# Kernel tuning notes

Measured on AMD Instinct MI355X. Metric: run time of the kernel, lower is better.

## Reference

```python
import jax, jax.numpy as jnp
import numpy as np

USER_COUNT = 100_000
ITEM_COUNT = 50_000
N_NODES = USER_COUNT + ITEM_COUNT
EMB = 128
N_LAYERS = 3
NNZ = 1_600_000
BATCH = 4096


def setup_inputs() -> dict:
    key = jax.random.key(0)
    k1, k2, k3, k4, k5 = jax.random.split(key, 5)
    # xavier-uniform-ish init scale for the embedding tables
    bound = float(np.sqrt(6.0 / (USER_COUNT + EMB)))
    user_emb = jax.random.uniform(k1, (USER_COUNT, EMB), jnp.float32, -bound, bound)
    bound_i = float(np.sqrt(6.0 / (ITEM_COUNT + EMB)))
    item_emb = jax.random.uniform(k2, (ITEM_COUNT, EMB), jnp.float32, -bound_i, bound_i)
    # random COO normalized adjacency (stand-in for scipy norm_adj)
    rng = np.random.default_rng(0)
    adj_rows = jnp.asarray(rng.integers(0, N_NODES, NNZ), dtype=jnp.int32)
    adj_cols = jnp.asarray(rng.integers(0, N_NODES, NNZ), dtype=jnp.int32)
    # values ~ 1/avg_degree so repeated SpMM stays numerically tame
    adj_vals = jnp.asarray(rng.random(NNZ, dtype=np.float32) * 0.1)
    users = jax.random.randint(k3, (BATCH,), 0, USER_COUNT, dtype=jnp.int64)
    items = jax.random.randint(k4, (BATCH,), 0, ITEM_COUNT, dtype=jnp.int64)
    return {
        "user_emb": user_emb,
        "item_emb": item_emb,
        "adj_vals": adj_vals,
        "adj_rows": adj_rows,
        "adj_cols": adj_cols,
        "users": users,
        "items": items,
    }


def _spmm(vals, rows, cols, x):
    # sparse [N,N] @ dense [N,D] via gather + segment_sum
    gathered = vals[:, None] * x[cols]  # [nnz, D]
    return jax.ops.segment_sum(gathered, rows, num_segments=N_NODES)


def reference(user_emb, item_emb, adj_vals, adj_rows, adj_cols, users, items):
    ego = jnp.concatenate([user_emb, item_emb], axis=0)  # [N, D]
    acc = ego  # running sum over layer outputs (fused stack+mean)
    for _ in range(N_LAYERS):
        ego = _spmm(adj_vals, adj_rows, adj_cols, ego)
        acc = acc + ego
    mean_emb = acc / (N_LAYERS + 1)
    user_out = mean_emb[users]
    item_out = mean_emb[USER_COUNT + items]
    return (user_out, item_out)
```

## Files before the change

kernel.cpp:

```cpp
#include <hip/hip_runtime.h>
#include <hip/hip_bf16.h>

#define USER_COUNT 100000
#define ITEM_COUNT 50000
#define N_NODES    (USER_COUNT + ITEM_COUNT)
#define EMB        128
#define NNZ        1600000
#define BATCH      4096

#define BSHIFT  10
#define BROWS   (1 << BSHIFT)
#define NBUCKET ((N_NODES + BROWS - 1) >> BSHIFT)
#define CAP     12288
#define TILE    4096

typedef unsigned int uint32;
typedef unsigned long long uint64;


__device__ __forceinline__ float bflo(uint32 p) { return __uint_as_float(p << 16); }
__device__ __forceinline__ float bfhi(uint32 p) { return __uint_as_float(p & 0xffff0000u); }
__device__ __forceinline__ uint32 bf16of(float a)
{
    uint32 u = __float_as_uint(a);
    return (u + 0x7fffu + ((u >> 16) & 1u)) >> 16;
}
__device__ __forceinline__ uint32 bf16pair(float a, float b)
{
    uint32 ua = __float_as_uint(a);
    uint32 ub = __float_as_uint(b);
    ua = (ua + 0x7fffu + ((ua >> 16) & 1u)) >> 16;
    ub = (ub + 0x7fffu + ((ub >> 16) & 1u)) & 0xffff0000u;
    return ua | ub;
}

__device__ __forceinline__ float dec14(uint32 rec)
{
    return __uint_as_float((((rec >> 28) + 108u) << 23) | (((rec >> 18) & 0x3FFu) << 13));
}
__device__ __forceinline__ uint32 enc14(uint32 b16)
{
    uint32 exp = (b16 >> 7) & 0xFFu;
    uint32 m7  = b16 & 0x7Fu;
    return (exp >= 108u) ? (((exp - 108u) << 10) | (m7 << 3)) : 0u;
}

__global__ void to_bf16(const float* __restrict__ user_emb,
                        const float* __restrict__ item_emb,
                        uint32* __restrict__ ego,
                        int* __restrict__ cursor,
                        uint32* __restrict__ mark)
{
    size_t t = (size_t)blockIdx.x * blockDim.x + threadIdx.x;
    if (t < NBUCKET) cursor[t] = 0;
    if (t < (N_NODES + 3) / 4) mark[t] = 0;
    size_t base = t * 8;
    if (base >= (size_t)N_NODES * EMB) return;
    const size_t user_elems = (size_t)USER_COUNT * EMB;
    const float* src = (base < user_elems) ? user_emb + base
                                           : item_emb + (base - user_elems);
    float4 a = *(const float4*)(src);
    float4 b = *(const float4*)(src + 4);
    uint32* dst = ego + base / 2;
    dst[0] = bf16pair(a.x, a.y);
    dst[1] = bf16pair(a.z, a.w);
    dst[2] = bf16pair(b.x, b.y);
    dst[3] = bf16pair(b.z, b.w);
}

__global__ __launch_bounds__(256)
void bin_coarse(const int* __restrict__ rows,
                const int* __restrict__ cols,
                const float* __restrict__ vals,
                int* __restrict__ cursor,
                uint64* __restrict__ binned)
{
    __shared__ int cnt[NBUCKET];
    __shared__ int offs[NBUCKET];
    __shared__ int base[NBUCKET];
    __shared__ int cur[NBUCKET];
    __shared__ int wsum[4];
    __shared__ uint64 stage[TILE];
    int t = threadIdx.x;
    int tileBase = blockIdx.x * TILE;
    int tileCount = min(TILE, NNZ - tileBase);

    for (int i = t; i < NBUCKET; i += 256) { cnt[i] = 0; cur[i] = 0; }
    __syncthreads();
    for (int i = t; i < tileCount; i += 256)
        atomicAdd(&cnt[rows[tileBase + i] >> BSHIFT], 1);
    __syncthreads();
    {
        int lane = t & 63, wid = t >> 6;
        int mine = (t < NBUCKET) ? cnt[t] : 0;
        int v = mine;
        #pragma unroll
        for (int off = 1; off <= 32; off <<= 1) {
            int u = __shfl_up(v, off, 64);
            if (lane >= off) v += u;
        }
        if (lane == 63) wsum[wid] = v;
        __syncthreads();
        int add = 0;
        for (int w = 0; w < wid; ++w) add += wsum[w];
        if (t < NBUCKET) offs[t] = v + add - mine;
    }
    if (t < NBUCKET) base[t] = atomicAdd(&cursor[t], cnt[t]);
    __syncthreads();
    for (int i = t; i < tileCount; i += 256) {
        int r = rows[tileBase + i];
        int c = cols[tileBase + i];
        float v = vals[tileBase + i];
        int b = r >> BSHIFT;
        int p = offs[b] + atomicAdd(&cur[b], 1);
        stage[p] = ((uint64)bf16of(v) << 36) | ((uint64)(uint32)r << 18) | (uint32)c;
    }
    __syncthreads();
    for (int i = t; i < tileCount; i += 256) {
        uint64 rec = stage[i];
        int r = (int)((rec >> 18) & 0x3FFFFu);
        int b = r >> BSHIFT;
        int dest = b * CAP + base[b] + (i - offs[b]);
        binned[dest] = rec;
    }
}

__global__ __launch_bounds__(1024)
void bin_fine(const int* __restrict__ cursor,
              const uint64* __restrict__ binned,
              uint32* __restrict__ row_info4,
              uint32* __restrict__ csr4)
{
    __shared__ int hist[BROWS];
    __shared__ int wsum[16];
    int b = blockIdx.x;
    int t = threadIdx.x;
    int lo = b * CAP;
    int hi = lo + cursor[b];

    hist[t] = 0;
    __syncthreads();
    for (int i = lo + t; i < hi; i += 1024) {
        int r = (int)((binned[i] >> 18) & 0x3FFFFu);
        atomicAdd(&hist[r & (BROWS - 1)], 1);
    }
    __syncthreads();
    int myVal = hist[t];
    int lane = t & 63, wid = t >> 6;
    int v = myVal;
    #pragma unroll
    for (int off = 1; off <= 32; off <<= 1) {
        int u = __shfl_up(v, off, 64);
        if (lane >= off) v += u;
    }
    if (lane == 63) wsum[wid] = v;
    __syncthreads();
    if (wid == 0 && lane < 16) {
        int s = wsum[lane];
        #pragma unroll
        for (int off = 1; off <= 8; off <<= 1) {
            int u = __shfl_up(s, off, 64);
            if (lane >= off) s += u;
        }
        wsum[lane] = s;
    }
    __syncthreads();
    int waveExcl = (wid == 0) ? 0 : wsum[wid - 1];
    int excl = waveExcl + v - myVal;
    int grow = (b << BSHIFT) + t;
    if (grow < N_NODES)
        row_info4[grow] = (uint32)(lo + excl) | ((uint32)myVal << 24);
    hist[t] = excl;
    __syncthreads();
    for (int i = lo + t; i < hi; i += 1024) {
        uint64 rec = binned[i];
        uint32 c = (uint32)(rec & 0x3FFFFu);
        int r = (int)((rec >> 18) & 0x3FFFFu);
        uint32 b16 = (uint32)(rec >> 36);
        int pos = lo + atomicAdd(&hist[r & (BROWS - 1)], 1);
        csr4[pos] = (enc14(b16) << 18) | c;
    }
}

__global__ void mark_needed(const uint32* __restrict__ row_info4,
                            const uint32* __restrict__ csr4,
                            const int* __restrict__ users,
                            const int* __restrict__ items,
                            unsigned char* __restrict__ mark)
{
    int b = blockIdx.x * blockDim.x + threadIdx.x;
    if (b >= 2 * BATCH) return;
    int node = (b < BATCH) ? users[b] : USER_COUNT + items[b - BATCH];
    mark[node] = 1;
    uint32 info = row_info4[node];
    int s = (int)(info & 0xFFFFFFu);
    int e = s + (int)(info >> 24);
    for (int k = s; k < e; ++k)
        mark[csr4[k] & 0x3FFFFu] = 1;
}

__global__ __launch_bounds__(256, 8)
void spmm_bf16(const uint32* __restrict__ row_info4,
               const uint32* __restrict__ csr4,
               const uint32* __restrict__ x,
               uint32* __restrict__ y)
{
    int half = threadIdx.x >> 5;
    int r = blockIdx.x * 8 + half;
    if (r >= N_NODES) return;
    int j = (threadIdx.x & 31) * 2;
    uint32 info = row_info4[r];
    int s = (int)(info & 0xFFFFFFu);
    int e = s + (int)(info >> 24);
    float4 acc = { 0.f, 0.f, 0.f, 0.f };
    for (int k = s; k < e; k += 4) {
        int i1 = (k + 1 < e) ? k + 1 : e - 1;
        int i2 = (k + 2 < e) ? k + 2 : e - 1;
        int i3 = (k + 3 < e) ? k + 3 : e - 1;
        uint32 r0 = csr4[k];
        uint32 r1 = csr4[i1];
        uint32 r2 = csr4[i2];
        uint32 r3 = csr4[i3];
        float v0 = dec14(r0);
        float v1 = (k + 1 < e) ? dec14(r1) : 0.f;
        float v2 = (k + 2 < e) ? dec14(r2) : 0.f;
        float v3 = (k + 3 < e) ? dec14(r3) : 0.f;
        uint2 g0 = *(const uint2*)(x + (size_t)(r0 & 0x3FFFFu) * (EMB / 2) + j);
        uint2 g1 = *(const uint2*)(x + (size_t)(r1 & 0x3FFFFu) * (EMB / 2) + j);
        uint2 g2 = *(const uint2*)(x + (size_t)(r2 & 0x3FFFFu) * (EMB / 2) + j);
        uint2 g3 = *(const uint2*)(x + (size_t)(r3 & 0x3FFFFu) * (EMB / 2) + j);
        acc.x += v0 * bflo(g0.x) + v1 * bflo(g1.x) + v2 * bflo(g2.x) + v3 * bflo(g3.x);
        acc.y += v0 * bfhi(g0.x) + v1 * bfhi(g1.x) + v2 * bfhi(g2.x) + v3 * bfhi(g3.x);
        acc.z += v0 * bflo(g0.y) + v1 * bflo(g1.y) + v2 * bflo(g2.y) + v3 * bflo(g3.y);
        acc.w += v0 * bfhi(g0.y) + v1 * bfhi(g1.y) + v2 * bfhi(g2.y) + v3 * bfhi(g3.y);
    }
    uint2 o;
    o.x = bf16pair(acc.x, acc.y);
    o.y = bf16pair(acc.z, acc.w);
    *(uint2*)(y + (size_t)r * (EMB / 2) + j) = o;
}

__global__ __launch_bounds__(256, 8)
void spmm_bf16_masked(const uint32* __restrict__ row_info4,
                      const uint32* __restrict__ csr4,
                      const uint32* __restrict__ x,
                      const unsigned char* __restrict__ mark,
                      uint32* __restrict__ y)
{
    int half = threadIdx.x >> 5;
    int r = blockIdx.x * 8 + half;
    if (r >= N_NODES) return;
    if (!mark[r]) return;
    int j = (threadIdx.x & 31) * 2;
    uint32 info = row_info4[r];
    int s = (int)(info & 0xFFFFFFu);
    int e = s + (int)(info >> 24);
    float4 acc = { 0.f, 0.f, 0.f, 0.f };
    for (int k = s; k < e; k += 4) {
        int i1 = (k + 1 < e) ? k + 1 : e - 1;
        int i2 = (k + 2 < e) ? k + 2 : e - 1;
        int i3 = (k + 3 < e) ? k + 3 : e - 1;
        uint32 r0 = csr4[k];
        uint32 r1 = csr4[i1];
        uint32 r2 = csr4[i2];
        uint32 r3 = csr4[i3];
        float v0 = dec14(r0);
        float v1 = (k + 1 < e) ? dec14(r1) : 0.f;
        float v2 = (k + 2 < e) ? dec14(r2) : 0.f;
        float v3 = (k + 3 < e) ? dec14(r3) : 0.f;
        uint2 g0 = *(const uint2*)(x + (size_t)(r0 & 0x3FFFFu) * (EMB / 2) + j);
        uint2 g1 = *(const uint2*)(x + (size_t)(r1 & 0x3FFFFu) * (EMB / 2) + j);
        uint2 g2 = *(const uint2*)(x + (size_t)(r2 & 0x3FFFFu) * (EMB / 2) + j);
        uint2 g3 = *(const uint2*)(x + (size_t)(r3 & 0x3FFFFu) * (EMB / 2) + j);
        acc.x += v0 * bflo(g0.x) + v1 * bflo(g1.x) + v2 * bflo(g2.x) + v3 * bflo(g3.x);
        acc.y += v0 * bfhi(g0.x) + v1 * bfhi(g1.x) + v2 * bfhi(g2.x) + v3 * bfhi(g3.x);
        acc.z += v0 * bflo(g0.y) + v1 * bflo(g1.y) + v2 * bflo(g2.y) + v3 * bflo(g3.y);
        acc.w += v0 * bfhi(g0.y) + v1 * bfhi(g1.y) + v2 * bfhi(g2.y) + v3 * bfhi(g3.y);
    }
    uint2 o;
    o.x = bf16pair(acc.x, acc.y);
    o.y = bf16pair(acc.z, acc.w);
    *(uint2*)(y + (size_t)r * (EMB / 2) + j) = o;
}

__global__ void spmm_final(const uint32* __restrict__ row_info4,
                           const uint32* __restrict__ csr4,
                           const uint32* __restrict__ buf0,
                           const uint32* __restrict__ buf1,
                           const float* __restrict__ user_emb,
                           const float* __restrict__ item_emb,
                           const int*   __restrict__ users,
                           const int*   __restrict__ items,
                           float* __restrict__ out)
{
    int half = threadIdx.x >> 5;
    int b = blockIdx.x * 8 + half;
    if (b >= 2 * BATCH) return;
    int node;
    const float* ego0;
    if (b < BATCH) {
        node = users[b];
        ego0 = user_emb + (size_t)node * EMB;
    } else {
        int it = items[b - BATCH];
        node = USER_COUNT + it;
        ego0 = item_emb + (size_t)it * EMB;
    }
    int j2 = (threadIdx.x & 31) * 2;
    int j4 = (threadIdx.x & 31) * 4;
    uint32 info = row_info4[node];
    int s = (int)(info & 0xFFFFFFu);
    int e = s + (int)(info >> 24);
    float4 acc = { 0.f, 0.f, 0.f, 0.f };
    for (int k = s; k < e; k += 4) {
        int i1 = (k + 1 < e) ? k + 1 : e - 1;
        int i2 = (k + 2 < e) ? k + 2 : e - 1;
        int i3 = (k + 3 < e) ? k + 3 : e - 1;
        uint32 r0 = csr4[k];
        uint32 r1 = csr4[i1];
        uint32 r2 = csr4[i2];
        uint32 r3 = csr4[i3];
        float v0 = dec14(r0);
        float v1 = (k + 1 < e) ? dec14(r1) : 0.f;
        float v2 = (k + 2 < e) ? dec14(r2) : 0.f;
        float v3 = (k + 3 < e) ? dec14(r3) : 0.f;
        uint2 g0 = *(const uint2*)(buf1 + (size_t)(r0 & 0x3FFFFu) * (EMB / 2) + j2);
        uint2 g1 = *(const uint2*)(buf1 + (size_t)(r1 & 0x3FFFFu) * (EMB / 2) + j2);
        uint2 g2 = *(const uint2*)(buf1 + (size_t)(r2 & 0x3FFFFu) * (EMB / 2) + j2);
        uint2 g3 = *(const uint2*)(buf1 + (size_t)(r3 & 0x3FFFFu) * (EMB / 2) + j2);
        acc.x += v0 * bflo(g0.x) + v1 * bflo(g1.x) + v2 * bflo(g2.x) + v3 * bflo(g3.x);
        acc.y += v0 * bfhi(g0.x) + v1 * bfhi(g1.x) + v2 * bfhi(g2.x) + v3 * bfhi(g3.x);
        acc.z += v0 * bflo(g0.y) + v1 * bflo(g1.y) + v2 * bflo(g2.y) + v3 * bflo(g3.y);
        acc.w += v0 * bfhi(g0.y) + v1 * bfhi(g1.y) + v2 * bfhi(g2.y) + v3 * bfhi(g3.y);
    }
    float4 a0 = *(const float4*)(ego0 + j4);
    uint2 b0 = *(const uint2*)(buf0 + (size_t)node * (EMB / 2) + j2);
    uint2 b1 = *(const uint2*)(buf1 + (size_t)node * (EMB / 2) + j2);
    float4 o;
    o.x = 0.25f * (a0.x + bflo(b0.x) + bflo(b1.x) + acc.x);
    o.y = 0.25f * (a0.y + bfhi(b0.x) + bfhi(b1.x) + acc.y);
    o.z = 0.25f * (a0.z + bflo(b0.y) + bflo(b1.y) + acc.z);
    o.w = 0.25f * (a0.w + bfhi(b0.y) + bfhi(b1.y) + acc.w);
    *(float4*)(out + (size_t)b * EMB + j4) = o;
}

extern "C" void kernel_launch(void* const* d_in, const int* in_sizes, int n_in,
                              void* d_out, int out_size, void* d_ws, size_t ws_size,
                              hipStream_t stream) {
    const float* user_emb = (const float*)d_in[0];
    const float* item_emb = (const float*)d_in[1];
    const float* adj_vals = (const float*)d_in[2];
    const int*   adj_rows = (const int*)d_in[3];
    const int*   adj_cols = (const int*)d_in[4];
    const int*   users    = (const int*)d_in[5];
    const int*   items    = (const int*)d_in[6];
    float* out = (float*)d_out;

    const size_t node_pairs = (size_t)N_NODES * (EMB / 2);
    char* p = (char*)d_ws;
    uint32* ego  = (uint32*)p;               p += node_pairs * sizeof(uint32);
    uint32* buf0 = (uint32*)p;               p += node_pairs * sizeof(uint32);
    uint32* buf1 = (uint32*)p;               p += node_pairs * sizeof(uint32);
    int* cursor       = (int*)p;             p += ((NBUCKET + 3) & ~3) * sizeof(int);
    uint32* mark      = (uint32*)p;          p += ((N_NODES + 63) & ~63);
    uint32* row_info4 = (uint32*)p;          p += (size_t)N_NODES * sizeof(uint32);
    uint64* binned    = (uint64*)p;          p += (size_t)NBUCKET * CAP * sizeof(uint64);
    uint32* csr4      = (uint32*)p;

    {
        size_t total = ((size_t)N_NODES * EMB) / 8;
        to_bf16<<<(int)((total + 255) / 256), 256, 0, stream>>>(
            user_emb, item_emb, ego, cursor, mark);
    }

    bin_coarse<<<(NNZ + TILE - 1) / TILE, 256, 0, stream>>>(
        adj_rows, adj_cols, adj_vals, cursor, binned);
    bin_fine<<<NBUCKET, 1024, 0, stream>>>(cursor, binned, row_info4, csr4);

    mark_needed<<<(2 * BATCH + 255) / 256, 256, 0, stream>>>(
        row_info4, csr4, users, items, (unsigned char*)mark);

    spmm_bf16<<<(N_NODES + 7) / 8, 256, 0, stream>>>(row_info4, csr4, ego, buf0);

    spmm_bf16_masked<<<(N_NODES + 7) / 8, 256, 0, stream>>>(
        row_info4, csr4, buf0, (const unsigned char*)mark, buf1);

    spmm_final<<<(2 * BATCH + 7) / 8, 256, 0, stream>>>(
        row_info4, csr4, buf0, buf1, user_emb, item_emb, users, items, out);
}
```

Baseline: 287.1 us.

## Fold needed-row marking into binning kernels and use nontemporal CSR loads/stores

Removes the separate mark_needed kernel. Batch nodes are now recorded in a bitmask inside bin_coarse, and bin_fine marks the neighbours of those rows while it scatters CSR entries. This saves one launch and a serial per-thread walk over neighbour lists. The SpMM kernels also switch to nontemporal loads for the CSR index and values, and nontemporal stores for their outputs, to reduce cache pollution. In exchange, bin_fine loads a ~19KB bitmask into shared memory per block, which may lower occupancy.

```diff
diff --git a/kernel.cpp b/kernel.cpp
--- a/kernel.cpp
+++ b/kernel.cpp
@@ -13,6 +13,7 @@
 #define NBUCKET ((N_NODES + BROWS - 1) >> BSHIFT)
 #define CAP     12288
 #define TILE    4096
+#define SELW    ((N_NODES + 31) / 32)
 
 typedef unsigned int uint32;
 typedef unsigned long long uint64;
@@ -49,11 +50,13 @@
                         const float* __restrict__ item_emb,
                         uint32* __restrict__ ego,
                         int* __restrict__ cursor,
-                        uint32* __restrict__ mark)
+                        uint32* __restrict__ mark,
+                        uint32* __restrict__ sel)
 {
     size_t t = (size_t)blockIdx.x * blockDim.x + threadIdx.x;
     if (t < NBUCKET) cursor[t] = 0;
     if (t < (N_NODES + 3) / 4) mark[t] = 0;
+    if (t < SELW) sel[t] = 0;
     size_t base = t * 8;
     if (base >= (size_t)N_NODES * EMB) return;
     const size_t user_elems = (size_t)USER_COUNT * EMB;
@@ -73,7 +76,11 @@
                 const int* __restrict__ cols,
                 const float* __restrict__ vals,
                 int* __restrict__ cursor,
-                uint64* __restrict__ binned)
+                uint64* __restrict__ binned,
+                const int* __restrict__ users,
+                const int* __restrict__ items,
+                uint32* __restrict__ sel,
+                unsigned char* __restrict__ mark)
 {
     __shared__ int cnt[NBUCKET];
     __shared__ int offs[NBUCKET];
@@ -84,6 +91,15 @@
     int t = threadIdx.x;
     int tileBase = blockIdx.x * TILE;
     int tileCount = min(TILE, NNZ - tileBase);
+
+    {
+        int gid = blockIdx.x * 256 + t;
+        if (gid < 2 * BATCH) {
+            int node = (gid < BATCH) ? users[gid] : USER_COUNT + items[gid - BATCH];
+            atomicOr(&sel[node >> 5], 1u << (node & 31));
+            mark[node] = 1;
+        }
+    }
 
     for (int i = t; i < NBUCKET; i += 256) { cnt[i] = 0; cur[i] = 0; }
     __syncthreads();
@@ -129,16 +145,20 @@
 void bin_fine(const int* __restrict__ cursor,
               const uint64* __restrict__ binned,
               uint32* __restrict__ row_info4,
-              uint32* __restrict__ csr4)
+              uint32* __restrict__ csr4,
+              const uint32* __restrict__ sel,
+              unsigned char* __restrict__ mark)
 {
     __shared__ int hist[BROWS];
     __shared__ int wsum[16];
+    __shared__ uint32 selS[SELW];
     int b = blockIdx.x;
     int t = threadIdx.x;
     int lo = b * CAP;
     int hi = lo + cursor[b];
 
     hist[t] = 0;
+    for (int i = t; i < SELW; i += 1024) selS[i] = sel[i];
     __syncthreads();
     for (int i = lo + t; i < hi; i += 1024) {
         int r = (int)((binned[i] >> 18) & 0x3FFFFu);
@@ -179,24 +199,9 @@
         uint32 b16 = (uint32)(rec >> 36);
         int pos = lo + atomicAdd(&hist[r & (BROWS - 1)], 1);
         csr4[pos] = (enc14(b16) << 18) | c;
-    }
-}
-
-__global__ void mark_needed(const uint32* __restrict__ row_info4,
-                            const uint32* __restrict__ csr4,
-                            const int* __restrict__ users,
-                            const int* __restrict__ items,
-                            unsigned char* __restrict__ mark)
-{
-    int b = blockIdx.x * blockDim.x + threadIdx.x;
-    if (b >= 2 * BATCH) return;
-    int node = (b < BATCH) ? users[b] : USER_COUNT + items[b - BATCH];
-    mark[node] = 1;
-    uint32 info = row_info4[node];
-    int s = (int)(info & 0xFFFFFFu);
-    int e = s + (int)(info >> 24);
-    for (int k = s; k < e; ++k)
-        mark[csr4[k] & 0x3FFFFu] = 1;
+        if ((selS[r >> 5] >> (r & 31)) & 1u)
+            mark[c] = 1;
+    }
 }
 
 __global__ __launch_bounds__(256, 8)
@@ -209,7 +214,7 @@
     int r = blockIdx.x * 8 + half;
     if (r >= N_NODES) return;
     int j = (threadIdx.x & 31) * 2;
-    uint32 info = row_info4[r];
+    uint32 info = __builtin_nontemporal_load(row_info4 + r);
     int s = (int)(info & 0xFFFFFFu);
     int e = s + (int)(info >> 24);
     float4 acc = { 0.f, 0.f, 0.f, 0.f };
@@ -217,10 +222,10 @@
         int i1 = (k + 1 < e) ? k + 1 : e - 1;
         int i2 = (k + 2 < e) ? k + 2 : e - 1;
         int i3 = (k + 3 < e) ? k + 3 : e - 1;
-        uint32 r0 = csr4[k];
-        uint32 r1 = csr4[i1];
-        uint32 r2 = csr4[i2];
-        uint32 r3 = csr4[i3];
+        uint32 r0 = __builtin_nontemporal_load(csr4 + k);
+        uint32 r1 = __builtin_nontemporal_load(csr4 + i1);
+        uint32 r2 = __builtin_nontemporal_load(csr4 + i2);
+        uint32 r3 = __builtin_nontemporal_load(csr4 + i3);
         float v0 = dec14(r0);
         float v1 = (k + 1 < e) ? dec14(r1) : 0.f;
         float v2 = (k + 2 < e) ? dec14(r2) : 0.f;
@@ -234,10 +239,9 @@
         acc.z += v0 * bflo(g0.y) + v1 * bflo(g1.y) + v2 * bflo(g2.y) + v3 * bflo(g3.y);
         acc.w += v0 * bfhi(g0.y) + v1 * bfhi(g1.y) + v2 * bfhi(g2.y) + v3 * bfhi(g3.y);
     }
-    uint2 o;
-    o.x = bf16pair(acc.x, acc.y);
-    o.y = bf16pair(acc.z, acc.w);
-    *(uint2*)(y + (size_t)r * (EMB / 2) + j) = o;
+    uint32* yp = y + (size_t)r * (EMB / 2) + j;
+    __builtin_nontemporal_store(bf16pair(acc.x, acc.y), yp);
+    __builtin_nontemporal_store(bf16pair(acc.z, acc.w), yp + 1);
 }
 
 __global__ __launch_bounds__(256, 8)
@@ -252,7 +256,7 @@
     if (r >= N_NODES) return;
     if (!mark[r]) return;
     int j = (threadIdx.x & 31) * 2;
-    uint32 info = row_info4[r];
+    uint32 info = __builtin_nontemporal_load(row_info4 + r);
     int s = (int)(info & 0xFFFFFFu);
     int e = s + (int)(info >> 24);
     float4 acc = { 0.f, 0.f, 0.f, 0.f };
@@ -260,10 +264,10 @@
         int i1 = (k + 1 < e) ? k + 1 : e - 1;
         int i2 = (k + 2 < e) ? k + 2 : e - 1;
         int i3 = (k + 3 < e) ? k + 3 : e - 1;
-        uint32 r0 = csr4[k];
-        uint32 r1 = csr4[i1];
-        uint32 r2 = csr4[i2];
-        uint32 r3 = csr4[i3];
+        uint32 r0 = __builtin_nontemporal_load(csr4 + k);
+        uint32 r1 = __builtin_nontemporal_load(csr4 + i1);
+        uint32 r2 = __builtin_nontemporal_load(csr4 + i2);
+        uint32 r3 = __builtin_nontemporal_load(csr4 + i3);
         float v0 = dec14(r0);
         float v1 = (k + 1 < e) ? dec14(r1) : 0.f;
         float v2 = (k + 2 < e) ? dec14(r2) : 0.f;
@@ -277,10 +281,9 @@
         acc.z += v0 * bflo(g0.y) + v1 * bflo(g1.y) + v2 * bflo(g2.y) + v3 * bflo(g3.y);
         acc.w += v0 * bfhi(g0.y) + v1 * bfhi(g1.y) + v2 * bfhi(g2.y) + v3 * bfhi(g3.y);
     }
-    uint2 o;
-    o.x = bf16pair(acc.x, acc.y);
-    o.y = bf16pair(acc.z, acc.w);
-    *(uint2*)(y + (size_t)r * (EMB / 2) + j) = o;
+    uint32* yp = y + (size_t)r * (EMB / 2) + j;
+    __builtin_nontemporal_store(bf16pair(acc.x, acc.y), yp);
+    __builtin_nontemporal_store(bf16pair(acc.z, acc.w), yp + 1);
 }
 
 __global__ void spmm_final(const uint32* __restrict__ row_info4,
@@ -308,7 +311,7 @@
     }
     int j2 = (threadIdx.x & 31) * 2;
     int j4 = (threadIdx.x & 31) * 4;
-    uint32 info = row_info4[node];
+    uint32 info = __builtin_nontemporal_load(row_info4 + node);
     int s = (int)(info & 0xFFFFFFu);
     int e = s + (int)(info >> 24);
     float4 acc = { 0.f, 0.f, 0.f, 0.f };
@@ -316,10 +319,10 @@
         int i1 = (k + 1 < e) ? k + 1 : e - 1;
         int i2 = (k + 2 < e) ? k + 2 : e - 1;
         int i3 = (k + 3 < e) ? k + 3 : e - 1;
-        uint32 r0 = csr4[k];
-        uint32 r1 = csr4[i1];
-        uint32 r2 = csr4[i2];
-        uint32 r3 = csr4[i3];
+        uint32 r0 = __builtin_nontemporal_load(csr4 + k);
+        uint32 r1 = __builtin_nontemporal_load(csr4 + i1);
+        uint32 r2 = __builtin_nontemporal_load(csr4 + i2);
+        uint32 r3 = __builtin_nontemporal_load(csr4 + i3);
         float v0 = dec14(r0);
         float v1 = (k + 1 < e) ? dec14(r1) : 0.f;
         float v2 = (k + 2 < e) ? dec14(r2) : 0.f;
@@ -363,6 +366,7 @@
     uint32* buf1 = (uint32*)p;               p += node_pairs * sizeof(uint32);
     int* cursor       = (int*)p;             p += ((NBUCKET + 3) & ~3) * sizeof(int);
     uint32* mark      = (uint32*)p;          p += ((N_NODES + 63) & ~63);
+    uint32* sel       = (uint32*)p;          p += SELW * sizeof(uint32);
     uint32* row_info4 = (uint32*)p;          p += (size_t)N_NODES * sizeof(uint32);
     uint64* binned    = (uint64*)p;          p += (size_t)NBUCKET * CAP * sizeof(uint64);
     uint32* csr4      = (uint32*)p;
@@ -370,15 +374,14 @@
     {
         size_t total = ((size_t)N_NODES * EMB) / 8;
         to_bf16<<<(int)((total + 255) / 256), 256, 0, stream>>>(
-            user_emb, item_emb, ego, cursor, mark);
+            user_emb, item_emb, ego, cursor, mark, sel);
     }
 
     bin_coarse<<<(NNZ + TILE - 1) / TILE, 256, 0, stream>>>(
-        adj_rows, adj_cols, adj_vals, cursor, binned);
-    bin_fine<<<NBUCKET, 1024, 0, stream>>>(cursor, binned, row_info4, csr4);
-
-    mark_needed<<<(2 * BATCH + 255) / 256, 256, 0, stream>>>(
-        row_info4, csr4, users, items, (unsigned char*)mark);
+        adj_rows, adj_cols, adj_vals, cursor, binned,
+        users, items, sel, (unsigned char*)mark);
+    bin_fine<<<NBUCKET, 1024, 0, stream>>>(
+        cursor, binned, row_info4, csr4, sel, (unsigned char*)mark);
 
     spmm_bf16<<<(N_NODES + 7) / 8, 256, 0, stream>>>(row_info4, csr4, ego, buf0);
 
```

New measurement: 308.3 us. 7.4% more time.

## Split SpMM feature columns into two half-row passes across separate blocks

Applied to the files above, without the earlier changes.

Each SpMM row is now processed by two blocks, each covering half of the 128-wide bf16 embedding, with 4-byte gathers instead of 8-byte gathers. The launch grid doubles so more wavefronts are in flight. The aim is to raise memory-level parallelism and cut per-thread register pressure. In exchange, the CSR index stream and row_info are read twice and each gather moves fewer bytes per request, which may raise instruction overhead.

```diff
diff --git a/kernel.cpp b/kernel.cpp
--- a/kernel.cpp
+++ b/kernel.cpp
@@ -13,6 +13,7 @@
 #define NBUCKET ((N_NODES + BROWS - 1) >> BSHIFT)
 #define CAP     12288
 #define TILE    4096
+#define NBLK    ((N_NODES + 7) / 8)
 
 typedef unsigned int uint32;
 typedef unsigned long long uint64;
@@ -205,14 +206,17 @@
                const uint32* __restrict__ x,
                uint32* __restrict__ y)
 {
+    int blk = blockIdx.x;
+    int pass = (blk >= NBLK) ? 1 : 0;
+    blk -= pass * NBLK;
     int half = threadIdx.x >> 5;
-    int r = blockIdx.x * 8 + half;
+    int r = blk * 8 + half;
     if (r >= N_NODES) return;
-    int j = (threadIdx.x & 31) * 2;
+    int j = (threadIdx.x & 31) + pass * 32;
     uint32 info = row_info4[r];
     int s = (int)(info & 0xFFFFFFu);
     int e = s + (int)(info >> 24);
-    float4 acc = { 0.f, 0.f, 0.f, 0.f };
+    float2 acc = { 0.f, 0.f };
     for (int k = s; k < e; k += 4) {
         int i1 = (k + 1 < e) ? k + 1 : e - 1;
         int i2 = (k + 2 < e) ? k + 2 : e - 1;
@@ -225,19 +229,14 @@
         float v1 = (k + 1 < e) ? dec14(r1) : 0.f;
         float v2 = (k + 2 < e) ? dec14(r2) : 0.f;
         float v3 = (k + 3 < e) ? dec14(r3) : 0.f;
-        uint2 g0 = *(const uint2*)(x + (size_t)(r0 & 0x3FFFFu) * (EMB / 2) + j);
-        uint2 g1 = *(const uint2*)(x + (size_t)(r1 & 0x3FFFFu) * (EMB / 2) + j);
-        uint2 g2 = *(const uint2*)(x + (size_t)(r2 & 0x3FFFFu) * (EMB / 2) + j);
-        uint2 g3 = *(const uint2*)(x + (size_t)(r3 & 0x3FFFFu) * (EMB / 2) + j);
-        acc.x += v0 * bflo(g0.x) + v1 * bflo(g1.x) + v2 * bflo(g2.x) + v3 * bflo(g3.x);
-        acc.y += v0 * bfhi(g0.x) + v1 * bfhi(g1.x) + v2 * bfhi(g2.x) + v3 * bfhi(g3.x);
-        acc.z += v0 * bflo(g0.y) + v1 * bflo(g1.y) + v2 * bflo(g2.y) + v3 * bflo(g3.y);
-        acc.w += v0 * bfhi(g0.y) + v1 * bfhi(g1.y) + v2 * bfhi(g2.y) + v3 * bfhi(g3.y);
-    }
-    uint2 o;
-    o.x = bf16pair(acc.x, acc.y);
-    o.y = bf16pair(acc.z, acc.w);
-    *(uint2*)(y + (size_t)r * (EMB / 2) + j) = o;
+        uint32 g0 = x[(size_t)(r0 & 0x3FFFFu) * (EMB / 2) + j];
+        uint32 g1 = x[(size_t)(r1 & 0x3FFFFu) * (EMB / 2) + j];
+        uint32 g2 = x[(size_t)(r2 & 0x3FFFFu) * (EMB / 2) + j];
+        uint32 g3 = x[(size_t)(r3 & 0x3FFFFu) * (EMB / 2) + j];
+        acc.x += v0 * bflo(g0) + v1 * bflo(g1) + v2 * bflo(g2) + v3 * bflo(g3);
+        acc.y += v0 * bfhi(g0) + v1 * bfhi(g1) + v2 * bfhi(g2) + v3 * bfhi(g3);
+    }
+    y[(size_t)r * (EMB / 2) + j] = bf16pair(acc.x, acc.y);
 }
 
 __global__ __launch_bounds__(256, 8)
@@ -247,15 +246,18 @@
                       const unsigned char* __restrict__ mark,
                       uint32* __restrict__ y)
 {
+    int blk = blockIdx.x;
+    int pass = (blk >= NBLK) ? 1 : 0;
+    blk -= pass * NBLK;
     int half = threadIdx.x >> 5;
-    int r = blockIdx.x * 8 + half;
+    int r = blk * 8 + half;
     if (r >= N_NODES) return;
     if (!mark[r]) return;
-    int j = (threadIdx.x & 31) * 2;
+    int j = (threadIdx.x & 31) + pass * 32;
     uint32 info = row_info4[r];
     int s = (int)(info & 0xFFFFFFu);
     int e = s + (int)(info >> 24);
-    float4 acc = { 0.f, 0.f, 0.f, 0.f };
+    float2 acc = { 0.f, 0.f };
     for (int k = s; k < e; k += 4) {
         int i1 = (k + 1 < e) ? k + 1 : e - 1;
         int i2 = (k + 2 < e) ? k + 2 : e - 1;
@@ -268,19 +270,14 @@
         float v1 = (k + 1 < e) ? dec14(r1) : 0.f;
         float v2 = (k + 2 < e) ? dec14(r2) : 0.f;
         float v3 = (k + 3 < e) ? dec14(r3) : 0.f;
-        uint2 g0 = *(const uint2*)(x + (size_t)(r0 & 0x3FFFFu) * (EMB / 2) + j);
-        uint2 g1 = *(const uint2*)(x + (size_t)(r1 & 0x3FFFFu) * (EMB / 2) + j);
-        uint2 g2 = *(const uint2*)(x + (size_t)(r2 & 0x3FFFFu) * (EMB / 2) + j);
-        uint2 g3 = *(const uint2*)(x + (size_t)(r3 & 0x3FFFFu) * (EMB / 2) + j);
-        acc.x += v0 * bflo(g0.x) + v1 * bflo(g1.x) + v2 * bflo(g2.x) + v3 * bflo(g3.x);
-        acc.y += v0 * bfhi(g0.x) + v1 * bfhi(g1.x) + v2 * bfhi(g2.x) + v3 * bfhi(g3.x);
-        acc.z += v0 * bflo(g0.y) + v1 * bflo(g1.y) + v2 * bflo(g2.y) + v3 * bflo(g3.y);
-        acc.w += v0 * bfhi(g0.y) + v1 * bfhi(g1.y) + v2 * bfhi(g2.y) + v3 * bfhi(g3.y);
-    }
-    uint2 o;
-    o.x = bf16pair(acc.x, acc.y);
-    o.y = bf16pair(acc.z, acc.w);
-    *(uint2*)(y + (size_t)r * (EMB / 2) + j) = o;
+        uint32 g0 = x[(size_t)(r0 & 0x3FFFFu) * (EMB / 2) + j];
+        uint32 g1 = x[(size_t)(r1 & 0x3FFFFu) * (EMB / 2) + j];
+        uint32 g2 = x[(size_t)(r2 & 0x3FFFFu) * (EMB / 2) + j];
+        uint32 g3 = x[(size_t)(r3 & 0x3FFFFu) * (EMB / 2) + j];
+        acc.x += v0 * bflo(g0) + v1 * bflo(g1) + v2 * bflo(g2) + v3 * bflo(g3);
+        acc.y += v0 * bfhi(g0) + v1 * bfhi(g1) + v2 * bfhi(g2) + v3 * bfhi(g3);
+    }
+    y[(size_t)r * (EMB / 2) + j] = bf16pair(acc.x, acc.y);
 }
 
 __global__ void spmm_final(const uint32* __restrict__ row_info4,
@@ -380,9 +377,9 @@
     mark_needed<<<(2 * BATCH + 255) / 256, 256, 0, stream>>>(
         row_info4, csr4, users, items, (unsigned char*)mark);
 
-    spmm_bf16<<<(N_NODES + 7) / 8, 256, 0, stream>>>(row_info4, csr4, ego, buf0);
-
-    spmm_bf16_masked<<<(N_NODES + 7) / 8, 256, 0, stream>>>(
+    spmm_bf16<<<2 * NBLK, 256, 0, stream>>>(row_info4, csr4, ego, buf0);
+
+    spmm_bf16_masked<<<2 * NBLK, 256, 0, stream>>>(
         row_info4, csr4, buf0, (const unsigned char*)mark, buf1);
 
     spmm_final<<<(2 * BATCH + 7) / 8, 256, 0, stream>>>(
```

New measurement: 321.7 us. 1.12x slower.

## Partition CSR rows by column half and cut gather unroll to two

Applied to the files above, without the earlier changes.

The fine binning pass now orders each row's nonzeros so that columns below a split point come first, and stores a per-row count of those low-column entries. The SpMM kernels process the two column ranges in separate passes, so concurrent waves tend to gather from the same half of the embedding table, which is meant to improve cache locality. The gather unroll also drops from four to two entries per iteration in all SpMM kernels. The costs are an extra shared histogram and atomics in binning and less memory-level parallelism per iteration.

```diff
diff --git a/kernel.cpp b/kernel.cpp
--- a/kernel.cpp
+++ b/kernel.cpp
@@ -13,6 +13,7 @@
 #define NBUCKET ((N_NODES + BROWS - 1) >> BSHIFT)
 #define CAP     12288
 #define TILE    4096
+#define CSPLIT  75000
 
 typedef unsigned int uint32;
 typedef unsigned long long uint64;
@@ -129,9 +130,11 @@
 void bin_fine(const int* __restrict__ cursor,
               const uint64* __restrict__ binned,
               uint32* __restrict__ row_info4,
+              unsigned char* __restrict__ cntlo,
               uint32* __restrict__ csr4)
 {
     __shared__ int hist[BROWS];
+    __shared__ int histlo[BROWS];
     __shared__ int wsum[16];
     int b = blockIdx.x;
     int t = threadIdx.x;
@@ -139,13 +142,18 @@
     int hi = lo + cursor[b];
 
     hist[t] = 0;
+    histlo[t] = 0;
     __syncthreads();
     for (int i = lo + t; i < hi; i += 1024) {
-        int r = (int)((binned[i] >> 18) & 0x3FFFFu);
+        uint64 rec = binned[i];
+        int r = (int)((rec >> 18) & 0x3FFFFu);
+        int c = (int)(rec & 0x3FFFFu);
         atomicAdd(&hist[r & (BROWS - 1)], 1);
+        if (c < CSPLIT) atomicAdd(&histlo[r & (BROWS - 1)], 1);
     }
     __syncthreads();
     int myVal = hist[t];
+    int myLo  = histlo[t];
     int lane = t & 63, wid = t >> 6;
     int v = myVal;
     #pragma unroll
@@ -168,16 +176,20 @@
     int waveExcl = (wid == 0) ? 0 : wsum[wid - 1];
     int excl = waveExcl + v - myVal;
     int grow = (b << BSHIFT) + t;
-    if (grow < N_NODES)
+    if (grow < N_NODES) {
         row_info4[grow] = (uint32)(lo + excl) | ((uint32)myVal << 24);
-    hist[t] = excl;
+        cntlo[grow] = (unsigned char)myLo;
+    }
+    hist[t]   = excl;
+    histlo[t] = excl + myLo;
     __syncthreads();
     for (int i = lo + t; i < hi; i += 1024) {
         uint64 rec = binned[i];
         uint32 c = (uint32)(rec & 0x3FFFFu);
         int r = (int)((rec >> 18) & 0x3FFFFu);
         uint32 b16 = (uint32)(rec >> 36);
-        int pos = lo + atomicAdd(&hist[r & (BROWS - 1)], 1);
+        int* ctr = (c < CSPLIT) ? &hist[r & (BROWS - 1)] : &histlo[r & (BROWS - 1)];
+        int pos = lo + atomicAdd(ctr, 1);
         csr4[pos] = (enc14(b16) << 18) | c;
     }
 }
@@ -199,8 +211,28 @@
         mark[csr4[k] & 0x3FFFFu] = 1;
 }
 
+__device__ __forceinline__ void spmm_run(const uint32* __restrict__ csr4,
+                                         const uint32* __restrict__ x,
+                                         int k0, int k1, int j, float4& acc)
+{
+    for (int k = k0; k < k1; k += 2) {
+        int i1 = (k + 1 < k1) ? k + 1 : k1 - 1;
+        uint32 r0 = csr4[k];
+        uint32 r1 = csr4[i1];
+        float v0 = dec14(r0);
+        float v1 = (k + 1 < k1) ? dec14(r1) : 0.f;
+        uint2 g0 = *(const uint2*)(x + (size_t)(r0 & 0x3FFFFu) * (EMB / 2) + j);
+        uint2 g1 = *(const uint2*)(x + (size_t)(r1 & 0x3FFFFu) * (EMB / 2) + j);
+        acc.x += v0 * bflo(g0.x) + v1 * bflo(g1.x);
+        acc.y += v0 * bfhi(g0.x) + v1 * bfhi(g1.x);
+        acc.z += v0 * bflo(g0.y) + v1 * bflo(g1.y);
+        acc.w += v0 * bfhi(g0.y) + v1 * bfhi(g1.y);
+    }
+}
+
 __global__ __launch_bounds__(256, 8)
 void spmm_bf16(const uint32* __restrict__ row_info4,
+               const unsigned char* __restrict__ cntlo,
                const uint32* __restrict__ csr4,
                const uint32* __restrict__ x,
                uint32* __restrict__ y)
@@ -212,28 +244,10 @@
     uint32 info = row_info4[r];
     int s = (int)(info & 0xFFFFFFu);
     int e = s + (int)(info >> 24);
+    int e1 = s + (int)cntlo[r];
     float4 acc = { 0.f, 0.f, 0.f, 0.f };
-    for (int k = s; k < e; k += 4) {
-        int i1 = (k + 1 < e) ? k + 1 : e - 1;
-        int i2 = (k + 2 < e) ? k + 2 : e - 1;
-        int i3 = (k + 3 < e) ? k + 3 : e - 1;
-        uint32 r0 = csr4[k];
-        uint32 r1 = csr4[i1];
-        uint32 r2 = csr4[i2];
-        uint32 r3 = csr4[i3];
-        float v0 = dec14(r0);
-        float v1 = (k + 1 < e) ? dec14(r1) : 0.f;
-        float v2 = (k + 2 < e) ? dec14(r2) : 0.f;
-        float v3 = (k + 3 < e) ? dec14(r3) : 0.f;
-        uint2 g0 = *(const uint2*)(x + (size_t)(r0 & 0x3FFFFu) * (EMB / 2) + j);
-        uint2 g1 = *(const uint2*)(x + (size_t)(r1 & 0x3FFFFu) * (EMB / 2) + j);
-        uint2 g2 = *(const uint2*)(x + (size_t)(r2 & 0x3FFFFu) * (EMB / 2) + j);
-        uint2 g3 = *(const uint2*)(x + (size_t)(r3 & 0x3FFFFu) * (EMB / 2) + j);
-        acc.x += v0 * bflo(g0.x) + v1 * bflo(g1.x) + v2 * bflo(g2.x) + v3 * bflo(g3.x);
-        acc.y += v0 * bfhi(g0.x) + v1 * bfhi(g1.x) + v2 * bfhi(g2.x) + v3 * bfhi(g3.x);
-        acc.z += v0 * bflo(g0.y) + v1 * bflo(g1.y) + v2 * bflo(g2.y) + v3 * bflo(g3.y);
-        acc.w += v0 * bfhi(g0.y) + v1 * bfhi(g1.y) + v2 * bfhi(g2.y) + v3 * bfhi(g3.y);
-    }
+    spmm_run(csr4, x, s, e1, j, acc);
+    spmm_run(csr4, x, e1, e, j, acc);
     uint2 o;
     o.x = bf16pair(acc.x, acc.y);
     o.y = bf16pair(acc.z, acc.w);
@@ -242,6 +256,7 @@
 
 __global__ __launch_bounds__(256, 8)
 void spmm_bf16_masked(const uint32* __restrict__ row_info4,
+                      const unsigned char* __restrict__ cntlo,
                       const uint32* __restrict__ csr4,
                       const uint32* __restrict__ x,
                       const unsigned char* __restrict__ mark,
@@ -255,28 +270,10 @@
     uint32 info = row_info4[r];
     int s = (int)(info & 0xFFFFFFu);
     int e = s + (int)(info >> 24);
+    int e1 = s + (int)cntlo[r];
     float4 acc = { 0.f, 0.f, 0.f, 0.f };
-    for (int k = s; k < e; k += 4) {
-        int i1 = (k + 1 < e) ? k + 1 : e - 1;
-        int i2 = (k + 2 < e) ? k + 2 : e - 1;
-        int i3 = (k + 3 < e) ? k + 3 : e - 1;
-        uint32 r0 = csr4[k];
-        uint32 r1 = csr4[i1];
-        uint32 r2 = csr4[i2];
-        uint32 r3 = csr4[i3];
-        float v0 = dec14(r0);
-        float v1 = (k + 1 < e) ? dec14(r1) : 0.f;
-        float v2 = (k + 2 < e) ? dec14(r2) : 0.f;
-        float v3 = (k + 3 < e) ? dec14(r3) : 0.f;
-        uint2 g0 = *(const uint2*)(x + (size_t)(r0 & 0x3FFFFu) * (EMB / 2) + j);
-        uint2 g1 = *(const uint2*)(x + (size_t)(r1 & 0x3FFFFu) * (EMB / 2) + j);
-        uint2 g2 = *(const uint2*)(x + (size_t)(r2 & 0x3FFFFu) * (EMB / 2) + j);
-        uint2 g3 = *(const uint2*)(x + (size_t)(r3 & 0x3FFFFu) * (EMB / 2) + j);
-        acc.x += v0 * bflo(g0.x) + v1 * bflo(g1.x) + v2 * bflo(g2.x) + v3 * bflo(g3.x);
-        acc.y += v0 * bfhi(g0.x) + v1 * bfhi(g1.x) + v2 * bfhi(g2.x) + v3 * bfhi(g3.x);
-        acc.z += v0 * bflo(g0.y) + v1 * bflo(g1.y) + v2 * bflo(g2.y) + v3 * bflo(g3.y);
-        acc.w += v0 * bfhi(g0.y) + v1 * bfhi(g1.y) + v2 * bfhi(g2.y) + v3 * bfhi(g3.y);
-    }
+    spmm_run(csr4, x, s, e1, j, acc);
+    spmm_run(csr4, x, e1, e, j, acc);
     uint2 o;
     o.x = bf16pair(acc.x, acc.y);
     o.y = bf16pair(acc.z, acc.w);
@@ -312,26 +309,18 @@
     int s = (int)(info & 0xFFFFFFu);
     int e = s + (int)(info >> 24);
     float4 acc = { 0.f, 0.f, 0.f, 0.f };
-    for (int k = s; k < e; k += 4) {
+    for (int k = s; k < e; k += 2) {
         int i1 = (k + 1 < e) ? k + 1 : e - 1;
-        int i2 = (k + 2 < e) ? k + 2 : e - 1;
-        int i3 = (k + 3 < e) ? k + 3 : e - 1;
         uint32 r0 = csr4[k];
         uint32 r1 = csr4[i1];
-        uint32 r2 = csr4[i2];
-        uint32 r3 = csr4[i3];
         float v0 = dec14(r0);
         float v1 = (k + 1 < e) ? dec14(r1) : 0.f;
-        float v2 = (k + 2 < e) ? dec14(r2) : 0.f;
-        float v3 = (k + 3 < e) ? dec14(r3) : 0.f;
         uint2 g0 = *(const uint2*)(buf1 + (size_t)(r0 & 0x3FFFFu) * (EMB / 2) + j2);
         uint2 g1 = *(const uint2*)(buf1 + (size_t)(r1 & 0x3FFFFu) * (EMB / 2) + j2);
-        uint2 g2 = *(const uint2*)(buf1 + (size_t)(r2 & 0x3FFFFu) * (EMB / 2) + j2);
-        uint2 g3 = *(const uint2*)(buf1 + (size_t)(r3 & 0x3FFFFu) * (EMB / 2) + j2);
-        acc.x += v0 * bflo(g0.x) + v1 * bflo(g1.x) + v2 * bflo(g2.x) + v3 * bflo(g3.x);
-        acc.y += v0 * bfhi(g0.x) + v1 * bfhi(g1.x) + v2 * bfhi(g2.x) + v3 * bfhi(g3.x);
-        acc.z += v0 * bflo(g0.y) + v1 * bflo(g1.y) + v2 * bflo(g2.y) + v3 * bflo(g3.y);
-        acc.w += v0 * bfhi(g0.y) + v1 * bfhi(g1.y) + v2 * bfhi(g2.y) + v3 * bfhi(g3.y);
+        acc.x += v0 * bflo(g0.x) + v1 * bflo(g1.x);
+        acc.y += v0 * bfhi(g0.x) + v1 * bfhi(g1.x);
+        acc.z += v0 * bflo(g0.y) + v1 * bflo(g1.y);
+        acc.w += v0 * bfhi(g0.y) + v1 * bfhi(g1.y);
     }
     float4 a0 = *(const float4*)(ego0 + j4);
     uint2 b0 = *(const uint2*)(buf0 + (size_t)node * (EMB / 2) + j2);
@@ -363,6 +352,7 @@
     uint32* buf1 = (uint32*)p;               p += node_pairs * sizeof(uint32);
     int* cursor       = (int*)p;             p += ((NBUCKET + 3) & ~3) * sizeof(int);
     uint32* mark      = (uint32*)p;          p += ((N_NODES + 63) & ~63);
+    unsigned char* cntlo = (unsigned char*)p; p += ((N_NODES + 63) & ~63);
     uint32* row_info4 = (uint32*)p;          p += (size_t)N_NODES * sizeof(uint32);
     uint64* binned    = (uint64*)p;          p += (size_t)NBUCKET * CAP * sizeof(uint64);
     uint32* csr4      = (uint32*)p;
@@ -375,15 +365,16 @@
 
     bin_coarse<<<(NNZ + TILE - 1) / TILE, 256, 0, stream>>>(
         adj_rows, adj_cols, adj_vals, cursor, binned);
-    bin_fine<<<NBUCKET, 1024, 0, stream>>>(cursor, binned, row_info4, csr4);
+    bin_fine<<<NBUCKET, 1024, 0, stream>>>(cursor, binned, row_info4, cntlo, csr4);
 
     mark_needed<<<(2 * BATCH + 255) / 256, 256, 0, stream>>>(
         row_info4, csr4, users, items, (unsigned char*)mark);
 
-    spmm_bf16<<<(N_NODES + 7) / 8, 256, 0, stream>>>(row_info4, csr4, ego, buf0);
+    spmm_bf16<<<(N_NODES + 7) / 8, 256, 0, stream>>>(
+        row_info4, cntlo, csr4, ego, buf0);
 
     spmm_bf16_masked<<<(N_NODES + 7) / 8, 256, 0, stream>>>(
-        row_info4, csr4, buf0, (const unsigned char*)mark, buf1);
+        row_info4, cntlo, csr4, buf0, (const unsigned char*)mark, buf1);
 
     spmm_final<<<(2 * BATCH + 7) / 8, 256, 0, stream>>>(
         row_info4, csr4, buf0, buf1, user_emb, item_emb, users, items, out);
```

After: 317.3 us. 10.5% more time.
